# Kernel tuning notes

Measured on AMD Instinct MI355X. Metric: run time of the kernel, lower is better.

The kernel has to match this reference:

```python
import jax, jax.numpy as jnp
import numpy as np


def setup_inputs() -> dict:
    key = jax.random.key(0)
    k1, k2, k3 = jax.random.split(key, 3)
    B, N, D, A = 64, 500000, 512, 7
    batch_rep = jax.random.normal(k1, (B, D), dtype=jnp.float32)
    representations = jax.random.normal(k2, (N, D), dtype=jnp.float32)
    actions = jax.random.normal(k3, (N, A), dtype=jnp.float32)
    return {
        "batch_rep": batch_rep,
        "representations": representations,
        "actions": actions,
        "k": 16,
    }


def reference(batch_rep, representations, actions, k):
    # torch.cdist (p=2): pairwise Euclidean distances [B, N] via the
    d2 = (
        jnp.sum(batch_rep * batch_rep, axis=1, keepdims=True)
        - 2.0 * (batch_rep @ representations.T)
        + jnp.sum(representations * representations, axis=1)[None, :]
    )
    dist = jnp.sqrt(jnp.maximum(d2, 0.0))  # [B, N]

    # torch.topk(largest=False): smallest-k distances == top-k of negated.
    neg_top, indices = jax.lax.top_k(-dist, k)  # [B, k]
    top_k_dist = -neg_top

    # weights = softmax(-dist) over the k neighbors
    weights = jax.nn.softmax(-top_k_dist, axis=1)  # [B, k]

    top_k_actions = actions[indices]  # gather -> [B, k, A]
    pred = jnp.sum(top_k_actions * weights[..., None], axis=1)  # [B, A]
    return pred, indices
```

## Files before the change

### kernel.cpp

```cpp
#include <hip/hip_runtime.h>
#include <stdint.h>

typedef _Float16 f16;
typedef _Float16 f16x8 __attribute__((ext_vector_type(8)));
typedef float f32x4 __attribute__((ext_vector_type(4)));

#define INF_F __builtin_inff()
#define INF_I 0x7fffffff
#define KM 24
#define SCALE 262144.0f

__device__ __forceinline__ bool lexLess(float s1, int n1, float s2, int n2) {
    return (s1 < s2) || (s1 == s2 && n1 < n2);
}
__device__ __forceinline__ bool lexLessI(int s1, int n1, int s2, int n2) {
    return (s1 < s2) || (s1 == s2 && n1 < n2);
}

__device__ __forceinline__ uint4 pack8(const float4 a, const float4 b) {
    const auto p0 = __builtin_amdgcn_cvt_pkrtz(a.x, a.y);
    const auto p1 = __builtin_amdgcn_cvt_pkrtz(a.z, a.w);
    const auto p2 = __builtin_amdgcn_cvt_pkrtz(b.x, b.y);
    const auto p3 = __builtin_amdgcn_cvt_pkrtz(b.z, b.w);
    uint4 u;
    u.x = __builtin_bit_cast(unsigned, p0);
    u.y = __builtin_bit_cast(unsigned, p1);
    u.z = __builtin_bit_cast(unsigned, p2);
    u.w = __builtin_bit_cast(unsigned, p3);
    return u;
}

__global__ __launch_bounds__(256, 4) void dist_topk_kernel(
    const float* __restrict__ reps, const float* __restrict__ brep,
    float* __restrict__ cs, int* __restrict__ ci,
    int N, int TT, int NBLK)
{
    __shared__ int slds[64][65];
    __shared__ int topdI[16][64];
    __shared__ int topiI[16][64];
    __shared__ int thrS[64], thrnS[64], cntS[64];

    const int tid = threadIdx.x;
    const int w = tid >> 6, lane = tid & 63;
    const int li = lane & 15, q = lane >> 4;
    const int b = blockIdx.x;

    uint4 a[4][4];
    #pragma unroll
    for (int ks = 0; ks < 4; ks++)
        #pragma unroll
        for (int mt = 0; mt < 4; mt++) {
            const float* src = brep + (mt * 16 + li) * 512 + 128 * w + 32 * ks + 8 * q;
            const float4 x0 = *(const float4*)(src);
            const float4 x1 = *(const float4*)(src + 4);
            a[ks][mt] = pack8(x0, x1);
        }

    if (tid < 64) { thrS[tid] = INF_I; thrnS[tid] = INF_I; cntS[tid] = 0; }
    for (int i = tid; i < 64 * 65; i += 256) ((int*)slds)[i] = 0;
    __syncthreads();

    int sc = 0;
    for (int t = b; t < TT; t += NBLK, sc++) {
        const int n0 = t * 64;

        #pragma unroll 1
        for (int nsub = 0; nsub < 4; nsub++) {
            const int rowl = n0 + nsub * 16 + li;
            const size_t rowc = (size_t)(rowl < N ? rowl : N - 1);
            const float* bp = reps + rowc * 512 + 128 * w + 8 * q;

            f32x4 acc0 = {0.f,0.f,0.f,0.f}, acc1 = {0.f,0.f,0.f,0.f};
            f32x4 acc2 = {0.f,0.f,0.f,0.f}, acc3 = {0.f,0.f,0.f,0.f};
            float yn = 0.f;

            float4 y0A = *(const float4*)(bp);
            float4 y1A = *(const float4*)(bp + 4);
            #pragma unroll
            for (int ks = 0; ks < 4; ks++) {
                float4 y0B, y1B;
                if (ks < 3) {
                    y0B = *(const float4*)(bp + (ks + 1) * 32);
                    y1B = *(const float4*)(bp + (ks + 1) * 32 + 4);
                }
                yn = fmaf(y0A.x, y0A.x, fmaf(y0A.y, y0A.y, fmaf(y0A.z, y0A.z, fmaf(y0A.w, y0A.w, yn))));
                yn = fmaf(y1A.x, y1A.x, fmaf(y1A.y, y1A.y, fmaf(y1A.z, y1A.z, fmaf(y1A.w, y1A.w, yn))));
                const f16x8 bf = __builtin_bit_cast(f16x8, pack8(y0A, y1A));
                acc0 = __builtin_amdgcn_mfma_f32_16x16x32_f16(__builtin_bit_cast(f16x8, a[ks][0]), bf, acc0, 0, 0, 0);
                acc1 = __builtin_amdgcn_mfma_f32_16x16x32_f16(__builtin_bit_cast(f16x8, a[ks][1]), bf, acc1, 0, 0, 0);
                acc2 = __builtin_amdgcn_mfma_f32_16x16x32_f16(__builtin_bit_cast(f16x8, a[ks][2]), bf, acc2, 0, 0, 0);
                acc3 = __builtin_amdgcn_mfma_f32_16x16x32_f16(__builtin_bit_cast(f16x8, a[ks][3]), bf, acc3, 0, 0, 0);
                if (ks < 3) { y0A = y0B; y1A = y1B; }
            }

            float ys = yn;
            ys += __shfl_xor(ys, 16);
            ys += __shfl_xor(ys, 32);
            const int nloc = nsub * 16 + li;
            if (q == 0) atomicAdd(&slds[nloc][64], __float2int_rn(ys * SCALE));
            #pragma unroll
            for (int jj = 0; jj < 4; jj++) {
                atomicAdd(&slds[nloc][ 0 + 4 * q + jj], __float2int_rn(acc0[jj] * SCALE));
                atomicAdd(&slds[nloc][16 + 4 * q + jj], __float2int_rn(acc1[jj] * SCALE));
                atomicAdd(&slds[nloc][32 + 4 * q + jj], __float2int_rn(acc2[jj] * SCALE));
                atomicAdd(&slds[nloc][48 + 4 * q + jj], __float2int_rn(acc3[jj] * SCALE));
            }
        }

        __syncthreads();

        if (w == (sc & 3)) {
            const int r = lane;
            const int* sb = &slds[0][0];
            int thr = thrS[r], thrn = thrnS[r], cnt = cntS[r];
            for (int j = 0; j < 64; j++) {
                const int n = n0 + j;
                if (n >= N) break;
                const int s = sb[j * 65 + 64] - 2 * sb[j * 65 + r];
                if (lexLessI(s, n, thr, thrn)) {
                    if (cnt < 16) {
                        topdI[cnt][r] = s; topiI[cnt][r] = n; cnt++;
                        if (cnt == 16) {
                            int tv = topdI[0][r], tn = topiI[0][r];
                            #pragma unroll
                            for (int u = 1; u < 16; u++) {
                                int v = topdI[u][r], nn = topiI[u][r];
                                if (!lexLessI(v, nn, tv, tn)) { tv = v; tn = nn; }
                            }
                            thr = tv; thrn = tn;
                        }
                    } else {
                        #pragma unroll
                        for (int u = 0; u < 16; u++)
                            if (topdI[u][r] == thr && topiI[u][r] == thrn) {
                                topdI[u][r] = s; topiI[u][r] = n; break;
                            }
                        int tv = topdI[0][r], tn = topiI[0][r];
                        #pragma unroll
                        for (int u = 1; u < 16; u++) {
                            int v = topdI[u][r], nn = topiI[u][r];
                            if (!lexLessI(v, nn, tv, tn)) { tv = v; tn = nn; }
                        }
                        thr = tv; thrn = tn;
                    }
                }
            }
            thrS[r] = thr; thrnS[r] = thrn; cntS[r] = cnt;
            for (int e2 = lane; e2 < 64 * 65; e2 += 64) (&slds[0][0])[e2] = 0;
        }

        __syncthreads();
    }

    __syncthreads();
    if (tid < 64) {
        const int c = cntS[tid];
        const size_t base = ((size_t)b * 64 + tid) * 16;
        for (int j = 0; j < 16; j++) {
            cs[base + j] = (j < c) ? ((float)topdI[j][tid] * (1.0f / SCALE)) : INF_F;
            ci[base + j] = (j < c) ? topiI[j][tid] : INF_I;
        }
    }
}

__global__ __launch_bounds__(256) void merge_kernel(
    const float* __restrict__ cs, const int* __restrict__ ci,
    const float* __restrict__ brep, const float* __restrict__ reps,
    const float* __restrict__ acts,
    float* __restrict__ out, int NLISTS, int N, int BA)
{
    const int r = blockIdx.x;
    const int tid = threadIdx.x;
    __shared__ __align__(16) float xrow[512];
    __shared__ float S1s[256 * KM];
    __shared__ int   S1i[256 * KM];
    __shared__ float S2s[32 * KM];
    __shared__ int   S2i[32 * KM];
    __shared__ double fd[KM];
    __shared__ int    fn[KM];

    if (tid < 128)
        *(float4*)(&xrow[tid * 4]) = *(const float4*)(&brep[(size_t)r * 512 + tid * 4]);

    float ls[KM]; int li[KM];
    #pragma unroll
    for (int j = 0; j < KM; j++) { ls[j] = INF_F; li[j] = INF_I; }
    float mv = INF_F; int mn = INF_I; int mp = 0;
    const int total = NLISTS * 16;
    for (int e = tid; e < total; e += 256) {
        const int blk = e >> 4, j = e & 15;
        const size_t a = (size_t)blk * 1024 + (size_t)r * 16 + j;
        const float s = cs[a]; const int n = ci[a];
        if (lexLess(s, n, mv, mn)) {
            ls[mp] = s; li[mp] = n;
            mv = ls[0]; mn = li[0]; mp = 0;
            #pragma unroll
            for (int u = 1; u < KM; u++)
                if (!lexLess(ls[u], li[u], mv, mn)) { mv = ls[u]; mn = li[u]; mp = u; }
        }
    }
    #pragma unroll
    for (int j = 0; j < KM; j++) { S1s[tid * KM + j] = ls[j]; S1i[tid * KM + j] = li[j]; }
    __syncthreads();

    if (tid < 32) {
        #pragma unroll
        for (int j = 0; j < KM; j++) { ls[j] = INF_F; li[j] = INF_I; }
        mv = INF_F; mn = INF_I; mp = 0;
        for (int e = tid * 8 * KM; e < (tid * 8 + 8) * KM; e++) {
            const float s = S1s[e]; const int n = S1i[e];
            if (lexLess(s, n, mv, mn)) {
                ls[mp] = s; li[mp] = n;
                mv = ls[0]; mn = li[0]; mp = 0;
                #pragma unroll
                for (int u = 1; u < KM; u++)
                    if (!lexLess(ls[u], li[u], mv, mn)) { mv = ls[u]; mn = li[u]; mp = u; }
            }
        }
        #pragma unroll
        for (int j = 0; j < KM; j++) { S2s[tid * KM + j] = ls[j]; S2i[tid * KM + j] = li[j]; }
    }
    __syncthreads();

    if (tid == 0) {
        #pragma unroll
        for (int j = 0; j < KM; j++) { ls[j] = INF_F; li[j] = INF_I; }
        mv = INF_F; mn = INF_I; mp = 0;
        for (int e = 0; e < 32 * KM; e++) {
            const float s = S2s[e]; const int n = S2i[e];
            if (lexLess(s, n, mv, mn)) {
                ls[mp] = s; li[mp] = n;
                mv = ls[0]; mn = li[0]; mp = 0;
                #pragma unroll
                for (int u = 1; u < KM; u++)
                    if (!lexLess(ls[u], li[u], mv, mn)) { mv = ls[u]; mn = li[u]; mp = u; }
            }
        }
        for (int j = 0; j < KM; j++) fn[j] = li[j];
    }
    __syncthreads();

    if (tid < KM) {
        const int n = fn[tid];
        double d = 1.0e300;
        if (n >= 0 && n < N) {
            d = 0.0;
            const float* yp = reps + (size_t)n * 512;
            for (int i = 0; i < 512; i += 4) {
                float4 yv = *(const float4*)(yp + i);
                double d0 = (double)xrow[i + 0] - (double)yv.x;
                double d1 = (double)xrow[i + 1] - (double)yv.y;
                double d2 = (double)xrow[i + 2] - (double)yv.z;
                double d3 = (double)xrow[i + 3] - (double)yv.w;
                d += d0 * d0 + d1 * d1 + d2 * d2 + d3 * d3;
            }
        }
        fd[tid] = d;
    }
    __syncthreads();

    if (tid == 0) {
        int ord[KM];
        for (int j = 0; j < KM; j++) ord[j] = j;
        for (int a = 0; a < 16; a++) {
            int best = a;
            for (int u = a + 1; u < KM; u++) {
                const int ou = ord[u], ob = ord[best];
                if (fd[ou] < fd[ob] || (fd[ou] == fd[ob] && fn[ou] < fn[ob])) best = u;
            }
            int tmp = ord[a]; ord[a] = ord[best]; ord[best] = tmp;
        }
        double dist[16];
        for (int j = 0; j < 16; j++) {
            double v = fd[ord[j]];
            dist[j] = sqrt(v > 0.0 ? v : 0.0);
        }
        double wv[16], wsum = 0.0;
        for (int j = 0; j < 16; j++) { wv[j] = exp(dist[0] - dist[j]); wsum += wv[j]; }
        for (int a = 0; a < 7; a++) {
            double s = 0.0;
            for (int j = 0; j < 16; j++)
                s += wv[j] * (double)acts[(size_t)fn[ord[j]] * 7 + a];
            out[r * 7 + a] = (float)(s / wsum);
        }
        for (int j = 0; j < 16; j++)
            out[BA + r * 16 + j] = (float)fn[ord[j]];
    }
}

extern "C" void kernel_launch(void* const* d_in, const int* in_sizes, int n_in,
                              void* d_out, int out_size, void* d_ws, size_t ws_size,
                              hipStream_t stream) {
    const float* brep = (const float*)d_in[0];
    const float* reps = (const float*)d_in[1];
    const float* acts = (const float*)d_in[2];
    const int D = 512;
    const int B = in_sizes[0] / D;
    const int N = in_sizes[1] / D;
    float* out = (float*)d_out;

    int NBLK = 1024;
    const size_t perblk = (size_t)64 * 16 * 8;
    while (NBLK > 1 && (size_t)NBLK * perblk > ws_size) NBLK >>= 1;

    float* cs = (float*)d_ws;
    int* ci = (int*)((char*)d_ws + (size_t)NBLK * 64 * 16 * 4);

    const int TT = (N + 63) / 64;

    dist_topk_kernel<<<NBLK, 256, 0, stream>>>(reps, brep, cs, ci, N, TT, NBLK);
    merge_kernel<<<B, 256, 0, stream>>>(cs, ci, brep, reps, acts, out, NBLK, N, B * 7);
}
```

Measured before the change: 1.249 ms.

## Double block to 512 threads, split K across 8 waves, prefetch next tile

Blocks grow from 256 to 512 threads, so each of 8 waves covers 64 of the 512 K elements and holds half as many A fragments in registers. The four 16-row sub-tiles are flattened into one unrolled 8-step loop that prefetches the next row chunk, crossing into the next tile at the boundary, to hide global-load latency. Grid size is halved to 512 blocks and the per-tile top-k update rotates over 8 waves. Each tile's result now needs twice as many LDS atomics, and there are fewer blocks in the grid.

New measurement: 1.470 ms. 17.7% more time.

```diff
diff --git a/kernel.cpp b/kernel.cpp
--- a/kernel.cpp
+++ b/kernel.cpp
@@ -30,7 +30,7 @@
     return u;
 }
 
-__global__ __launch_bounds__(256, 4) void dist_topk_kernel(
+__global__ __launch_bounds__(512, 4) void dist_topk_kernel(
     const float* __restrict__ reps, const float* __restrict__ brep,
     float* __restrict__ cs, int* __restrict__ ci,
     int N, int TT, int NBLK)
@@ -44,72 +44,83 @@
     const int w = tid >> 6, lane = tid & 63;
     const int li = lane & 15, q = lane >> 4;
     const int b = blockIdx.x;
-
-    uint4 a[4][4];
+    const int kbase = 64 * w + 8 * q;
+
+    uint4 a[2][4];
     #pragma unroll
-    for (int ks = 0; ks < 4; ks++)
+    for (int ks2 = 0; ks2 < 2; ks2++)
         #pragma unroll
         for (int mt = 0; mt < 4; mt++) {
-            const float* src = brep + (mt * 16 + li) * 512 + 128 * w + 32 * ks + 8 * q;
+            const float* src = brep + (mt * 16 + li) * 512 + kbase + 32 * ks2;
             const float4 x0 = *(const float4*)(src);
             const float4 x1 = *(const float4*)(src + 4);
-            a[ks][mt] = pack8(x0, x1);
+            a[ks2][mt] = pack8(x0, x1);
         }
 
     if (tid < 64) { thrS[tid] = INF_I; thrnS[tid] = INF_I; cntS[tid] = 0; }
-    for (int i = tid; i < 64 * 65; i += 256) ((int*)slds)[i] = 0;
-    __syncthreads();
+    for (int i = tid; i < 64 * 65; i += 512) ((int*)slds)[i] = 0;
+    __syncthreads();
+
+    float4 yA0, yA1;
+    {
+        const int r0 = min(b * 64 + li, N - 1);
+        const float* p = reps + (size_t)r0 * 512 + kbase;
+        yA0 = *(const float4*)(p);
+        yA1 = *(const float4*)(p + 4);
+    }
 
     int sc = 0;
     for (int t = b; t < TT; t += NBLK, sc++) {
         const int n0 = t * 64;
 
-        #pragma unroll 1
-        for (int nsub = 0; nsub < 4; nsub++) {
-            const int rowl = n0 + nsub * 16 + li;
-            const size_t rowc = (size_t)(rowl < N ? rowl : N - 1);
-            const float* bp = reps + rowc * 512 + 128 * w + 8 * q;
-
-            f32x4 acc0 = {0.f,0.f,0.f,0.f}, acc1 = {0.f,0.f,0.f,0.f};
-            f32x4 acc2 = {0.f,0.f,0.f,0.f}, acc3 = {0.f,0.f,0.f,0.f};
-            float yn = 0.f;
-
-            float4 y0A = *(const float4*)(bp);
-            float4 y1A = *(const float4*)(bp + 4);
-            #pragma unroll
-            for (int ks = 0; ks < 4; ks++) {
-                float4 y0B, y1B;
-                if (ks < 3) {
-                    y0B = *(const float4*)(bp + (ks + 1) * 32);
-                    y1B = *(const float4*)(bp + (ks + 1) * 32 + 4);
+        f32x4 acc0, acc1, acc2, acc3;
+        float yn = 0.f;
+
+        #pragma unroll
+        for (int s = 0; s < 8; s++) {
+            const int nsub = s >> 1, ks2 = s & 1;
+            float4 yB0, yB1;
+            {
+                int nt0, ns;
+                if (s < 7) { nt0 = n0; ns = s + 1; }
+                else       { nt0 = min(t + NBLK, TT - 1) * 64; ns = 0; }
+                const int rr = min(nt0 + (ns >> 1) * 16 + li, N - 1);
+                const float* p = reps + (size_t)rr * 512 + kbase + 32 * (ns & 1);
+                yB0 = *(const float4*)(p);
+                yB1 = *(const float4*)(p + 4);
+            }
+            if (ks2 == 0) {
+                acc0 = (f32x4){0.f,0.f,0.f,0.f}; acc1 = (f32x4){0.f,0.f,0.f,0.f};
+                acc2 = (f32x4){0.f,0.f,0.f,0.f}; acc3 = (f32x4){0.f,0.f,0.f,0.f};
+                yn = 0.f;
+            }
+            yn = fmaf(yA0.x, yA0.x, fmaf(yA0.y, yA0.y, fmaf(yA0.z, yA0.z, fmaf(yA0.w, yA0.w, yn))));
+            yn = fmaf(yA1.x, yA1.x, fmaf(yA1.y, yA1.y, fmaf(yA1.z, yA1.z, fmaf(yA1.w, yA1.w, yn))));
+            const f16x8 bf = __builtin_bit_cast(f16x8, pack8(yA0, yA1));
+            acc0 = __builtin_amdgcn_mfma_f32_16x16x32_f16(__builtin_bit_cast(f16x8, a[ks2][0]), bf, acc0, 0, 0, 0);
+            acc1 = __builtin_amdgcn_mfma_f32_16x16x32_f16(__builtin_bit_cast(f16x8, a[ks2][1]), bf, acc1, 0, 0, 0);
+            acc2 = __builtin_amdgcn_mfma_f32_16x16x32_f16(__builtin_bit_cast(f16x8, a[ks2][2]), bf, acc2, 0, 0, 0);
+            acc3 = __builtin_amdgcn_mfma_f32_16x16x32_f16(__builtin_bit_cast(f16x8, a[ks2][3]), bf, acc3, 0, 0, 0);
+            if (ks2 == 1) {
+                float ys = yn;
+                ys += __shfl_xor(ys, 16);
+                ys += __shfl_xor(ys, 32);
+                const int nloc = nsub * 16 + li;
+                if (q == 0) atomicAdd(&slds[nloc][64], __float2int_rn(ys * SCALE));
+                #pragma unroll
+                for (int jj = 0; jj < 4; jj++) {
+                    atomicAdd(&slds[nloc][ 0 + 4 * q + jj], __float2int_rn(acc0[jj] * SCALE));
+                    atomicAdd(&slds[nloc][16 + 4 * q + jj], __float2int_rn(acc1[jj] * SCALE));
+                    atomicAdd(&slds[nloc][32 + 4 * q + jj], __float2int_rn(acc2[jj] * SCALE));
+                    atomicAdd(&slds[nloc][48 + 4 * q + jj], __float2int_rn(acc3[jj] * SCALE));
                 }
-                yn = fmaf(y0A.x, y0A.x, fmaf(y0A.y, y0A.y, fmaf(y0A.z, y0A.z, fmaf(y0A.w, y0A.w, yn))));
-                yn = fmaf(y1A.x, y1A.x, fmaf(y1A.y, y1A.y, fmaf(y1A.z, y1A.z, fmaf(y1A.w, y1A.w, yn))));
-                const f16x8 bf = __builtin_bit_cast(f16x8, pack8(y0A, y1A));
-                acc0 = __builtin_amdgcn_mfma_f32_16x16x32_f16(__builtin_bit_cast(f16x8, a[ks][0]), bf, acc0, 0, 0, 0);
-                acc1 = __builtin_amdgcn_mfma_f32_16x16x32_f16(__builtin_bit_cast(f16x8, a[ks][1]), bf, acc1, 0, 0, 0);
-                acc2 = __builtin_amdgcn_mfma_f32_16x16x32_f16(__builtin_bit_cast(f16x8, a[ks][2]), bf, acc2, 0, 0, 0);
-                acc3 = __builtin_amdgcn_mfma_f32_16x16x32_f16(__builtin_bit_cast(f16x8, a[ks][3]), bf, acc3, 0, 0, 0);
-                if (ks < 3) { y0A = y0B; y1A = y1B; }
-            }
-
-            float ys = yn;
-            ys += __shfl_xor(ys, 16);
-            ys += __shfl_xor(ys, 32);
-            const int nloc = nsub * 16 + li;
-            if (q == 0) atomicAdd(&slds[nloc][64], __float2int_rn(ys * SCALE));
-            #pragma unroll
-            for (int jj = 0; jj < 4; jj++) {
-                atomicAdd(&slds[nloc][ 0 + 4 * q + jj], __float2int_rn(acc0[jj] * SCALE));
-                atomicAdd(&slds[nloc][16 + 4 * q + jj], __float2int_rn(acc1[jj] * SCALE));
-                atomicAdd(&slds[nloc][32 + 4 * q + jj], __float2int_rn(acc2[jj] * SCALE));
-                atomicAdd(&slds[nloc][48 + 4 * q + jj], __float2int_rn(acc3[jj] * SCALE));
-            }
+            }
+            yA0 = yB0; yA1 = yB1;
         }
 
         __syncthreads();
 
-        if (w == (sc & 3)) {
+        if (w == (sc & 7)) {
             const int r = lane;
             const int* sb = &slds[0][0];
             int thr = thrS[r], thrn = thrnS[r], cnt = cntS[r];
@@ -299,7 +310,7 @@
     const int N = in_sizes[1] / D;
     float* out = (float*)d_out;
 
-    int NBLK = 1024;
+    int NBLK = 512;
     const size_t perblk = (size_t)64 * 16 * 8;
     while (NBLK > 1 && (size_t)NBLK * perblk > ws_size) NBLK >>= 1;
 
@@ -308,6 +319,6 @@
 
     const int TT = (N + 63) / 64;
 
-    dist_topk_kernel<<<NBLK, 256, 0, stream>>>(reps, brep, cs, ci, N, TT, NBLK);
+    dist_topk_kernel<<<NBLK, 512, 0, stream>>>(reps, brep, cs, ci, N, TT, NBLK);
     merge_kernel<<<B, 256, 0, stream>>>(cs, ci, brep, reps, acts, out, NBLK, N, B * 7);
 }
```

## Double-buffer LDS score tiles so top-k scan overlaps next tile's MFMA

Applied to the files above, without the earlier changes.

Splits the shared score buffer into two 32-row halves and shrinks each tile from 64 to 32 rows. The wave assigned to the scan now processes the previous tile while all waves compute and atomically accumulate the current one. This removes one of the two block barriers per iteration and hides the serial top-k insertion behind the GEMM work. It also switches to waves_per_eu and splits the fp64 rerank accumulation into four chains for more ILP. Smaller tiles mean more loop iterations and barrier overhead, and the scan leaves idle the wave that runs it.

Result: slower. 1.299 ms (+4.0%).

```diff
diff --git a/kernel.cpp b/kernel.cpp
--- a/kernel.cpp
+++ b/kernel.cpp
@@ -30,12 +30,14 @@
     return u;
 }
 
-__global__ __launch_bounds__(256, 4) void dist_topk_kernel(
+__global__ __launch_bounds__(256)
+__attribute__((amdgpu_waves_per_eu(4, 4)))
+void dist_topk_kernel(
     const float* __restrict__ reps, const float* __restrict__ brep,
     float* __restrict__ cs, int* __restrict__ ci,
     int N, int TT, int NBLK)
 {
-    __shared__ int slds[64][65];
+    __shared__ int slds[2][32][65];
     __shared__ int topdI[16][64];
     __shared__ int topiI[16][64];
     __shared__ int thrS[64], thrnS[64], cntS[64];
@@ -57,16 +59,58 @@
         }
 
     if (tid < 64) { thrS[tid] = INF_I; thrnS[tid] = INF_I; cntS[tid] = 0; }
-    for (int i = tid; i < 64 * 65; i += 256) ((int*)slds)[i] = 0;
-    __syncthreads();
+    for (int i = tid; i < 2 * 32 * 65; i += 256) ((int*)slds)[i] = 0;
+    __syncthreads();
+
+    auto scan = [&](int scp) {
+        const long n0p = ((long)b + (long)scp * NBLK) * 32;
+        const int r = lane;
+        volatile int* sb = &slds[scp & 1][0][0];
+        int thr = thrS[r], thrn = thrnS[r], cnt = cntS[r];
+        for (int j = 0; j < 32; j++) {
+            const long n = n0p + j;
+            if (n >= N) break;
+            const int s = sb[j * 65 + 64] - 2 * sb[j * 65 + r];
+            if (lexLessI(s, (int)n, thr, thrn)) {
+                if (cnt < 16) {
+                    topdI[cnt][r] = s; topiI[cnt][r] = (int)n; cnt++;
+                    if (cnt == 16) {
+                        int tv = topdI[0][r], tn = topiI[0][r];
+                        #pragma unroll
+                        for (int u = 1; u < 16; u++) {
+                            int v = topdI[u][r], nn = topiI[u][r];
+                            if (!lexLessI(v, nn, tv, tn)) { tv = v; tn = nn; }
+                        }
+                        thr = tv; thrn = tn;
+                    }
+                } else {
+                    #pragma unroll
+                    for (int u = 0; u < 16; u++)
+                        if (topdI[u][r] == thr && topiI[u][r] == thrn) {
+                            topdI[u][r] = s; topiI[u][r] = (int)n; break;
+                        }
+                    int tv = topdI[0][r], tn = topiI[0][r];
+                    #pragma unroll
+                    for (int u = 1; u < 16; u++) {
+                        int v = topdI[u][r], nn = topiI[u][r];
+                        if (!lexLessI(v, nn, tv, tn)) { tv = v; tn = nn; }
+                    }
+                    thr = tv; thrn = tn;
+                }
+            }
+        }
+        thrS[r] = thr; thrnS[r] = thrn; cntS[r] = cnt;
+        for (int e2 = lane; e2 < 32 * 65; e2 += 64) sb[e2] = 0;
+    };
 
     int sc = 0;
-    for (int t = b; t < TT; t += NBLK, sc++) {
-        const int n0 = t * 64;
+    for (long t = b; t < (long)TT; t += NBLK, sc++) {
+        const int p = sc & 1;
+        const long n0 = t * 32;
 
         #pragma unroll 1
-        for (int nsub = 0; nsub < 4; nsub++) {
-            const int rowl = n0 + nsub * 16 + li;
+        for (int nsub = 0; nsub < 2; nsub++) {
+            const long rowl = n0 + nsub * 16 + li;
             const size_t rowc = (size_t)(rowl < N ? rowl : N - 1);
             const float* bp = reps + rowc * 512 + 128 * w + 8 * q;
 
@@ -97,62 +141,27 @@
             ys += __shfl_xor(ys, 16);
             ys += __shfl_xor(ys, 32);
             const int nloc = nsub * 16 + li;
-            if (q == 0) atomicAdd(&slds[nloc][64], __float2int_rn(ys * SCALE));
+            if (q == 0) atomicAdd(&slds[p][nloc][64], __float2int_rn(ys * SCALE));
             #pragma unroll
             for (int jj = 0; jj < 4; jj++) {
-                atomicAdd(&slds[nloc][ 0 + 4 * q + jj], __float2int_rn(acc0[jj] * SCALE));
-                atomicAdd(&slds[nloc][16 + 4 * q + jj], __float2int_rn(acc1[jj] * SCALE));
-                atomicAdd(&slds[nloc][32 + 4 * q + jj], __float2int_rn(acc2[jj] * SCALE));
-                atomicAdd(&slds[nloc][48 + 4 * q + jj], __float2int_rn(acc3[jj] * SCALE));
-            }
-        }
-
-        __syncthreads();
-
-        if (w == (sc & 3)) {
-            const int r = lane;
-            const int* sb = &slds[0][0];
-            int thr = thrS[r], thrn = thrnS[r], cnt = cntS[r];
-            for (int j = 0; j < 64; j++) {
-                const int n = n0 + j;
-                if (n >= N) break;
-                const int s = sb[j * 65 + 64] - 2 * sb[j * 65 + r];
-                if (lexLessI(s, n, thr, thrn)) {
-                    if (cnt < 16) {
-                        topdI[cnt][r] = s; topiI[cnt][r] = n; cnt++;
-                        if (cnt == 16) {
-                            int tv = topdI[0][r], tn = topiI[0][r];
-                            #pragma unroll
-                            for (int u = 1; u < 16; u++) {
-                                int v = topdI[u][r], nn = topiI[u][r];
-                                if (!lexLessI(v, nn, tv, tn)) { tv = v; tn = nn; }
-                            }
-                            thr = tv; thrn = tn;
-                        }
-                    } else {
-                        #pragma unroll
-                        for (int u = 0; u < 16; u++)
-                            if (topdI[u][r] == thr && topiI[u][r] == thrn) {
-                                topdI[u][r] = s; topiI[u][r] = n; break;
-                            }
-                        int tv = topdI[0][r], tn = topiI[0][r];
-                        #pragma unroll
-                        for (int u = 1; u < 16; u++) {
-                            int v = topdI[u][r], nn = topiI[u][r];
-                            if (!lexLessI(v, nn, tv, tn)) { tv = v; tn = nn; }
-                        }
-                        thr = tv; thrn = tn;
-                    }
-                }
-            }
-            thrS[r] = thr; thrnS[r] = thrn; cntS[r] = cnt;
-            for (int e2 = lane; e2 < 64 * 65; e2 += 64) (&slds[0][0])[e2] = 0;
-        }
-
-        __syncthreads();
-    }
-
-    __syncthreads();
+                atomicAdd(&slds[p][nloc][ 0 + 4 * q + jj], __float2int_rn(acc0[jj] * SCALE));
+                atomicAdd(&slds[p][nloc][16 + 4 * q + jj], __float2int_rn(acc1[jj] * SCALE));
+                atomicAdd(&slds[p][nloc][32 + 4 * q + jj], __float2int_rn(acc2[jj] * SCALE));
+                atomicAdd(&slds[p][nloc][48 + 4 * q + jj], __float2int_rn(acc3[jj] * SCALE));
+            }
+        }
+
+        if (sc > 0 && w == ((sc - 1) & 3)) scan(sc - 1);
+
+        asm volatile("s_waitcnt lgkmcnt(0)");
+        __builtin_amdgcn_sched_barrier(0);
+        __builtin_amdgcn_s_barrier();
+        __builtin_amdgcn_sched_barrier(0);
+    }
+
+    if (sc > 0 && w == ((sc - 1) & 3)) scan(sc - 1);
+    __syncthreads();
+
     if (tid < 64) {
         const int c = cntS[tid];
         const size_t base = ((size_t)b * 64 + tid) * 16;
@@ -244,16 +253,17 @@
         const int n = fn[tid];
         double d = 1.0e300;
         if (n >= 0 && n < N) {
-            d = 0.0;
+            double d0a = 0.0, d1a = 0.0, d2a = 0.0, d3a = 0.0;
             const float* yp = reps + (size_t)n * 512;
             for (int i = 0; i < 512; i += 4) {
                 float4 yv = *(const float4*)(yp + i);
-                double d0 = (double)xrow[i + 0] - (double)yv.x;
-                double d1 = (double)xrow[i + 1] - (double)yv.y;
-                double d2 = (double)xrow[i + 2] - (double)yv.z;
-                double d3 = (double)xrow[i + 3] - (double)yv.w;
-                d += d0 * d0 + d1 * d1 + d2 * d2 + d3 * d3;
-            }
+                double e0 = (double)xrow[i + 0] - (double)yv.x;
+                double e1 = (double)xrow[i + 1] - (double)yv.y;
+                double e2 = (double)xrow[i + 2] - (double)yv.z;
+                double e3 = (double)xrow[i + 3] - (double)yv.w;
+                d0a += e0 * e0; d1a += e1 * e1; d2a += e2 * e2; d3a += e3 * e3;
+            }
+            d = (d0a + d1a) + (d2a + d3a);
         }
         fd[tid] = d;
     }
@@ -306,7 +316,7 @@
     float* cs = (float*)d_ws;
     int* ci = (int*)((char*)d_ws + (size_t)NBLK * 64 * 16 * 4);
 
-    const int TT = (N + 63) / 64;
+    const int TT = (N + 31) / 32;
 
     dist_topk_kernel<<<NBLK, 256, 0, stream>>>(reps, brep, cs, ci, N, TT, NBLK);
     merge_kernel<<<B, 256, 0, stream>>>(cs, ci, brep, reps, acts, out, NBLK, N, B * 7);
```
